# Performance work log

Hardware: AMD Instinct MI355X
Metric: run time of the kernel (lower is better)

The kernel has to match this reference:

```python
import jax, jax.numpy as jnp
import numpy as np

MEAN_LOG = 0.0
STD_LOG = 1.0
D = 32          # context_size (SRU hidden)
K = 64          # num_mix_components
H = 3 * K       # MLP hidden width
LOG_2PI = float(np.log(2.0 * np.pi))


def clamp_preserve_gradients(x, lo, hi):
    # forward clamp, straight-through gradient
    return x + jax.lax.stop_gradient(jnp.clip(x, lo, hi) - x)


def setup_inputs() -> dict:
    key = jax.random.key(0)
    ks = jax.random.split(key, 10)
    B, S = 128, 4096
    inter_times = jax.random.uniform(ks[0], (B, S), dtype=jnp.float32)
    mask = jnp.ones((B, S), dtype=jnp.float32)
    ages_u = jax.random.uniform(ks[1], (B, S), dtype=jnp.float32)
    # SRU parameters (input_size=1, hidden=D, k=4 since 1 != D)
    W = jax.random.normal(ks[2], (1, 4 * D), dtype=jnp.float32) / np.sqrt(1.0)
    v = 0.1 * jax.random.normal(ks[3], (2 * D,), dtype=jnp.float32)   # weight_c (v_f, v_r)
    b = jnp.zeros((2 * D,), dtype=jnp.float32)                         # bias (b_f, b_r)
    context_init = jnp.zeros((D,), dtype=jnp.float32)
    # MLP: (D+1) -> H -> H -> H
    W1 = jax.random.normal(ks[4], (D + 1, H), dtype=jnp.float32) / np.sqrt(D + 1)
    b1 = jnp.zeros((H,), dtype=jnp.float32)
    W2 = jax.random.normal(ks[5], (H, H), dtype=jnp.float32) / np.sqrt(H)
    b2 = jnp.zeros((H,), dtype=jnp.float32)
    W3 = jax.random.normal(ks[6], (H, H), dtype=jnp.float32) / np.sqrt(H)
    b3 = jnp.zeros((H,), dtype=jnp.float32)
    return dict(inter_times=inter_times, mask=mask, ages_u=ages_u, W=W, v=v, b=b,
                context_init=context_init, W1=W1, b1=b1, W2=W2, b2=b2, W3=W3, b3=b3)


def reference(inter_times, mask, ages_u, W, v, b, context_init, W1, b1, W2, b2, W3, b3):
    B, S = inter_times.shape
    # --- features: normalized log inter-event times ---
    feats = (jnp.log(inter_times + 1e-8) - MEAN_LOG) / STD_LOG        # (B,S)
    x = feats[..., None]                                              # (B,S,1)
    # --- SRU: one big input projection, then elementwise recurrence via scan ---
    U = (x @ W).reshape(B, S, 4, D)                                   # (B,S,4,D)
    U = jnp.transpose(U, (1, 0, 2, 3))                                # (S,B,4,D) time-major
    vf, vr = v[:D], v[D:]
    bf, br = b[:D], b[D:]

    def step(c, u):
        u0, u1, u2, u3 = u[:, 0], u[:, 1], u[:, 2], u[:, 3]
        f = jax.nn.sigmoid(u1 + vf * c + bf)
        c_new = f * c + (1.0 - f) * u0
        r = jax.nn.sigmoid(u2 + vr * c_new + br)
        h = r * c_new + (1.0 - r) * u3                                # highway (identity activation)
        return c_new, h

    c0 = jnp.zeros((B, D), dtype=feats.dtype)
    _, hs = jax.lax.scan(step, c0, U)                                 # (S,B,D)
    context = jnp.transpose(hs, (1, 0, 2))                            # (B,S,D)
    # remove_last: shift right, prepend learned init context
    context = jnp.concatenate(
        [jnp.broadcast_to(context_init, (B, 1, D)), context[:, :-1, :]], axis=1)
    # --- age features / residual times ---
    ages = inter_times - inter_times * ages_u                         # elapsed age
    residual_times = inter_times - ages                               # = inter_times * ages_u
    ages_f = (jnp.log(ages + 1e-8) - MEAN_LOG) / STD_LOG
    ctx = jnp.concatenate([context, ages_f[..., None]], axis=-1)      # (B,S,D+1)
    # --- mixture-parameter MLP ---
    h1 = jax.nn.relu(ctx @ W1 + b1)
    h2 = jax.nn.relu(h1 @ W2 + b2)
    raw = h2 @ W3 + b3                                                # (B,S,3K)
    locs = raw[..., :K]
    log_scales = clamp_preserve_gradients(raw[..., K:2 * K], -5.0, 3.0)
    log_w = jax.nn.log_softmax(raw[..., 2 * K:], axis=-1)
    # --- log-normal mixture log-prob ---
    t = jnp.clip(residual_times, 1e-10, None)
    y = jnp.log(t)
    z = (y - MEAN_LOG) / STD_LOG
    zs = (z[..., None] - locs) * jnp.exp(-log_scales)
    comp = log_w - log_scales - 0.5 * LOG_2PI - 0.5 * zs * zs         # (B,S,K)
    log_p = jax.scipy.special.logsumexp(comp, axis=-1) - jnp.log(STD_LOG) - y
    log_p = log_p * mask
    return log_p.sum(-1)                                              # (B,)
```

## Files before the change

### kernel.cpp

```cpp
#include <hip/hip_runtime.h>
#include <hip/hip_bf16.h>
#include <math.h>
#include <type_traits>

#define Bn 128
#define Sn 4096
#define Dn 32
#define Hn 192
#define ASTR 196
#define CH 32
#define CHL 128
#define BURN 128
#define HALF_LOG2PI 0.9189385332046727f

typedef __attribute__((ext_vector_type(8))) short short8v;
typedef __attribute__((ext_vector_type(4))) float f32x4;

__device__ __forceinline__ unsigned short f2bf(float x) {
    return (unsigned short)((__float_as_uint(x) + 0x8000u) >> 16);
}
__device__ __forceinline__ float bf2f(unsigned short u) {
    return __uint_as_float(((unsigned)u) << 16);
}
__device__ __forceinline__ unsigned pack_bf2(float lo, float hi) {
    __hip_bfloat162 h = __float22bfloat162_rn(float2{lo, hi});
    return *reinterpret_cast<unsigned*>(&h);
}

__global__ __launch_bounds__(64) void pack_weights(
    const float* __restrict__ W1, const float* __restrict__ W2,
    const float* __restrict__ W3, unsigned short* __restrict__ wp)
{
    int fid = blockIdx.x, lane = threadIdx.x;
    const float* Wsrc; int Krows, f;
    if (fid < 24)      { Wsrc = W1; Krows = 33;  f = fid; }
    else if (fid < 96) { Wsrc = W2; Krows = 192; f = fid - 24; }
    else               { Wsrc = W3; Krows = 192; f = fid - 96; }
    int kstep = f / 12, nb = f % 12;
    int k0 = kstep * 32 + 8 * (lane >> 4);
    int n  = nb * 16 + (lane & 15);
    short8v v;
#pragma unroll
    for (int j = 0; j < 8; ++j) {
        int k = k0 + j;
        float x = (k < Krows) ? Wsrc[k * Hn + n] : 0.0f;
        v[j] = (short)f2bf(x);
    }
    *(short8v*)(wp + (size_t)fid * 512 + lane * 8) = v;
}

__global__ __launch_bounds__(256) void recurrence_kernel(
    const float* __restrict__ it_g, const float* __restrict__ W,
    const float* __restrict__ v,    const float* __restrict__ bia,
    const float* __restrict__ cinit, unsigned short* __restrict__ ctx)
{
    const float LOG2E = 1.4426950408889634f;
    int g = blockIdx.x * 256 + threadIdx.x;
    int d = g & 31;
    int bc = g >> 5;
    int b = bc & (Bn - 1);
    int chunk = bc >> 7;

    float w0 = W[d], w3 = W[96 + d];
    float nw1l = -W[32 + d] * LOG2E, nw2l = -W[64 + d] * LOG2E;
    float nvfl = -v[d] * LOG2E,      nvrl = -v[32 + d] * LOG2E;
    float nbfl = -bia[d] * LOG2E,    nbrl = -bia[32 + d] * LOG2E;

    const f32x4* itv = (const f32x4*)(it_g + (size_t)b * Sn);
    unsigned short* cp = ctx + ((size_t)b * Sn) * Dn + d;
    int s_start = chunk * CHL;
    int s_end   = s_start + CHL;
    int sbeg    = (chunk == 0) ? 0 : s_start - BURN;
    if (chunk == 0) cp[0] = f2bf(cinit[d]);

    float c = 0.0f;
    int blk0 = sbeg >> 3, blkN = s_end >> 3;
    f32x4 A0 = itv[blk0 * 2], A1 = itv[blk0 * 2 + 1];
    for (int blk = blk0; blk < blkN; ++blk) {
        f32x4 N0 = A0, N1 = A1;
        if (blk + 1 < blkN) { N0 = itv[blk * 2 + 2]; N1 = itv[blk * 2 + 3]; }
        float feat[8];
#pragma unroll
        for (int j = 0; j < 4; ++j) {
            feat[j]     = __logf(A0[j] + 1e-8f);
            feat[j + 4] = __logf(A1[j] + 1e-8f);
        }
        unsigned short hb[8];
#pragma unroll
        for (int j = 0; j < 8; ++j) {
            float ft = feat[j];
            float u0 = ft * w0, u3 = ft * w3;
            float nxfl = fmaf(ft, nw1l, nbfl);
            float nxrl = fmaf(ft, nw2l, nbrl);
            float sfn = fmaf(nvfl, c, nxfl);
            float ef  = __builtin_amdgcn_exp2f(sfn);
            float f_  = __builtin_amdgcn_rcpf(1.0f + ef);
            float cmu = c - u0;
            float cn  = fmaf(f_, cmu, u0);
            float srn = fmaf(nvrl, cn, nxrl);
            float er  = __builtin_amdgcn_exp2f(srn);
            float r_  = __builtin_amdgcn_rcpf(1.0f + er);
            float h   = fmaf(r_, cn - u3, u3);
            c = cn;
            hb[j] = f2bf(h);
        }
        int s0 = blk * 8;
        if (s0 >= s_start) {
#pragma unroll
            for (int j = 0; j < 8; ++j)
                if (s0 + j + 1 < Sn) cp[(size_t)(s0 + j + 1) * Dn] = hb[j];
        }
        A0 = N0; A1 = N1;
    }
}

__global__ __launch_bounds__(128, 2) void mlp_kernel(
    const float* __restrict__ it_g, const float* __restrict__ mask_g,
    const float* __restrict__ au_g, const unsigned short* __restrict__ ctxb,
    const unsigned short* __restrict__ wp,
    const float* __restrict__ b1, const float* __restrict__ b2,
    const float* __restrict__ b3, float* __restrict__ out)
{
    __shared__ __align__(16) unsigned short Acts[64 * ASTR];
    __shared__ float wsum[2];

    const int tid = threadIdx.x;
    const int lane = tid & 63;
    const int wv = tid >> 6;
    const int gq = lane >> 4;
    const int cl = lane & 15;
    const long tile = (long)blockIdx.x * 64;
    const int b = (int)(tile >> 12);
    const int nbase = wv * 6;

    {
        int tok = tid >> 1, h = tid & 1;
        unsigned short* row = Acts + tok * ASTR;
        const unsigned short* src = ctxb + (tile + tok) * Dn + h * 16;
        *(short8v*)(row + h * 16)     = *(const short8v*)src;
        *(short8v*)(row + h * 16 + 8) = *(const short8v*)(src + 8);
        short8v z = {0, 0, 0, 0, 0, 0, 0, 0};
        if (h == 0) {
            float itv = it_g[tile + tok];
            float auv = au_g[tile + tok];
            short8v za = z;
            za[0] = (short)f2bf(__logf(fmaf(-auv, itv, itv) + 1e-8f));
            *(short8v*)(row + 32) = za;
        } else {
            *(short8v*)(row + 40) = z;
            *(short8v*)(row + 48) = z;
            *(short8v*)(row + 56) = z;
        }
    }
    __syncthreads();

    f32x4 acc[6][4];

    auto run_layer = [&](auto NKC, const unsigned short* wpl,
                         const float* __restrict__ bias) {
        constexpr int nk = NKC.value;
#pragma unroll
        for (int j = 0; j < 6; ++j) {
            f32x4 bb = *(const f32x4*)(bias + (nbase + j) * 16 + 4 * gq);
#pragma unroll
            for (int m = 0; m < 4; ++m) acc[j][m] = bb;
        }
#pragma unroll
        for (int ks = 0; ks < nk; ++ks) {
            short8v bfv[4];
#pragma unroll
            for (int m = 0; m < 4; ++m)
                bfv[m] = *(const short8v*)(Acts + (m * 16 + cl) * ASTR + ks * 32 + 8 * gq);
            const unsigned short* wk = wpl + ((size_t)ks * 12 + nbase) * 512 + lane * 8;
#pragma unroll
            for (int j = 0; j < 6; ++j) {
                short8v af = *(const short8v*)(wk + j * 512);
#pragma unroll
                for (int m = 0; m < 4; ++m)
                    acc[j][m] = __builtin_amdgcn_mfma_f32_16x16x32_bf16(af, bfv[m], acc[j][m], 0, 0, 0);
            }
        }
    };

    auto store_h = [&](bool relu) {
#pragma unroll
        for (int j = 0; j < 6; ++j) {
            int fbase = (nbase + j) * 16 + 4 * gq;
#pragma unroll
            for (int m = 0; m < 4; ++m) {
                f32x4 vv = acc[j][m];
                if (relu) {
#pragma unroll
                    for (int r = 0; r < 4; ++r) vv[r] = fmaxf(vv[r], 0.0f);
                }
                uint2 pk;
                pk.x = pack_bf2(vv[0], vv[1]);
                pk.y = pack_bf2(vv[2], vv[3]);
                *(uint2*)(Acts + (m * 16 + cl) * ASTR + fbase) = pk;
            }
        }
    };

    run_layer(std::integral_constant<int, 2>{}, wp, b1);
    __syncthreads();
    store_h(true);
    __syncthreads();
    run_layer(std::integral_constant<int, 6>{}, wp + 24 * 512, b2);
    __syncthreads();
    store_h(true);
    __syncthreads();
    run_layer(std::integral_constant<int, 6>{}, wp + 96 * 512, b3);
    __syncthreads();
    store_h(false);
    __syncthreads();

    float psum = 0.0f;
#pragma unroll
    for (int pass = 0; pass < 2; ++pass) {
        int t = lane >> 2;
        int cpart = lane & 3;
        int rowi = wv * 32 + pass * 16 + t;
        long tok = tile + rowi;
        const unsigned short* rowp = Acts + rowi * ASTR + 16 * cpart;

        short8v L0 = *(const short8v*)(rowp);
        short8v L1 = *(const short8v*)(rowp + 8);
        short8v S0 = *(const short8v*)(rowp + 64);
        short8v S1 = *(const short8v*)(rowp + 72);
        short8v G0 = *(const short8v*)(rowp + 128);
        short8v G1 = *(const short8v*)(rowp + 136);

        float itv = it_g[tok];
        float auv = au_g[tok];
        float mk  = mask_g[tok];
        float y = __logf(fmaxf(itv * auv, 1e-10f));

        float lg[16];
#pragma unroll
        for (int i = 0; i < 8; ++i) {
            lg[i]     = bf2f((unsigned short)G0[i]);
            lg[8 + i] = bf2f((unsigned short)G1[i]);
        }
        float m1 = lg[0];
#pragma unroll
        for (int i = 1; i < 16; ++i) m1 = fmaxf(m1, lg[i]);
        m1 = fmaxf(m1, __shfl_xor(m1, 1, 64));
        m1 = fmaxf(m1, __shfl_xor(m1, 2, 64));

        float sa = 0.0f, sb = 0.0f;
#pragma unroll
        for (int i = 0; i < 16; ++i) {
            float loc = bf2f((unsigned short)(i < 8 ? L0[i] : L1[i - 8]));
            float lsr = bf2f((unsigned short)(i < 8 ? S0[i] : S1[i - 8]));
            lsr = fminf(fmaxf(lsr, -5.0f), 3.0f);
            float zs = (y - loc) * __expf(-lsr);
            float g = -lsr - HALF_LOG2PI - 0.5f * zs * zs;
            sa += __expf(lg[i] - m1);
            sb += __expf(lg[i] - m1 + g);
        }
        sa += __shfl_xor(sa, 1, 64); sa += __shfl_xor(sa, 2, 64);
        sb += __shfl_xor(sb, 1, 64); sb += __shfl_xor(sb, 2, 64);

        float lp = (__logf(sb) - __logf(sa) - y) * mk;
        if (cpart == 0) psum += lp;
    }
#pragma unroll
    for (int mm = 4; mm < 64; mm <<= 1) psum += __shfl_xor(psum, mm, 64);
    psum += __shfl_xor(psum, 1, 64);
    psum += __shfl_xor(psum, 2, 64);
    if (lane == 0) wsum[wv] = psum;
    __syncthreads();
    if (tid == 0) atomicAdd(out + b, wsum[0] + wsum[1]);
}

extern "C" void kernel_launch(void* const* d_in, const int* in_sizes, int n_in,
                              void* d_out, int out_size, void* d_ws, size_t ws_size,
                              hipStream_t stream) {
    const float* it_g  = (const float*)d_in[0];
    const float* mask  = (const float*)d_in[1];
    const float* au    = (const float*)d_in[2];
    const float* W     = (const float*)d_in[3];
    const float* v     = (const float*)d_in[4];
    const float* bia   = (const float*)d_in[5];
    const float* cinit = (const float*)d_in[6];
    const float* W1    = (const float*)d_in[7];
    const float* b1    = (const float*)d_in[8];
    const float* W2    = (const float*)d_in[9];
    const float* b2    = (const float*)d_in[10];
    const float* W3    = (const float*)d_in[11];
    const float* b3    = (const float*)d_in[12];
    float* out = (float*)d_out;

    unsigned short* ctxb = (unsigned short*)d_ws;
    unsigned short* wp   = ctxb + (size_t)Bn * Sn * Dn;

    hipMemsetAsync(d_out, 0, (size_t)out_size * sizeof(float), stream);

    pack_weights<<<168, 64, 0, stream>>>(W1, W2, W3, wp);
    recurrence_kernel<<<(Bn * Dn * CH) / 256, 256, 0, stream>>>(
        it_g, W, v, bia, cinit, ctxb);
    mlp_kernel<<<(Bn * Sn) / 64, 128, 0, stream>>>(
        it_g, mask, au, ctxb, wp, b1, b2, b3, out);
}
```

Measured before the change: 194.1 us.

## Compute mixture log-prob epilogue directly from layer-3 MFMA accumulators

Layer 3's output columns are reassigned across the two waves so each wave holds matching loc, log-scale and weight blocks for the same 32 mixture components in registers. The log-sum-exp then runs straight from the fp32 accumulators, and only the per-wave partial results are merged through a small LDS exchange. This removes the bf16 store of layer-3 outputs to LDS, the barriers around it and the reload. As a side effect, the final mixture parameters are no longer rounded to bf16. The cost is more register pressure and a two-way log-sum-exp merge.

Result: faster. 186.0 us (-4.2%).

```diff
diff --git a/kernel.cpp b/kernel.cpp
--- a/kernel.cpp
+++ b/kernel.cpp
@@ -18,9 +18,6 @@
 
 __device__ __forceinline__ unsigned short f2bf(float x) {
     return (unsigned short)((__float_as_uint(x) + 0x8000u) >> 16);
-}
-__device__ __forceinline__ float bf2f(unsigned short u) {
-    return __uint_as_float(((unsigned)u) << 16);
 }
 __device__ __forceinline__ unsigned pack_bf2(float lo, float hi) {
     __hip_bfloat162 h = __float22bfloat162_rn(float2{lo, hi});
@@ -131,7 +128,8 @@
     const int cl = lane & 15;
     const long tile = (long)blockIdx.x * 64;
     const int b = (int)(tile >> 12);
-    const int nbase = wv * 6;
+
+#define NBM(j) ((j) + (((j) >= 2) ? 2 : 0) + (((j) >= 4) ? 2 : 0) + 2 * wv)
 
     {
         int tok = tid >> 1, h = tid & 1;
@@ -161,7 +159,7 @@
         constexpr int nk = NKC.value;
 #pragma unroll
         for (int j = 0; j < 6; ++j) {
-            f32x4 bb = *(const f32x4*)(bias + (nbase + j) * 16 + 4 * gq);
+            f32x4 bb = *(const f32x4*)(bias + NBM(j) * 16 + 4 * gq);
 #pragma unroll
             for (int m = 0; m < 4; ++m) acc[j][m] = bb;
         }
@@ -171,10 +169,10 @@
 #pragma unroll
             for (int m = 0; m < 4; ++m)
                 bfv[m] = *(const short8v*)(Acts + (m * 16 + cl) * ASTR + ks * 32 + 8 * gq);
-            const unsigned short* wk = wpl + ((size_t)ks * 12 + nbase) * 512 + lane * 8;
+            const unsigned short* wk = wpl + (size_t)ks * (12 * 512) + lane * 8;
 #pragma unroll
             for (int j = 0; j < 6; ++j) {
-                short8v af = *(const short8v*)(wk + j * 512);
+                short8v af = *(const short8v*)(wk + NBM(j) * 512);
 #pragma unroll
                 for (int m = 0; m < 4; ++m)
                     acc[j][m] = __builtin_amdgcn_mfma_f32_16x16x32_bf16(af, bfv[m], acc[j][m], 0, 0, 0);
@@ -182,17 +180,15 @@
         }
     };
 
-    auto store_h = [&](bool relu) {
+    auto store_h = [&]() {
 #pragma unroll
         for (int j = 0; j < 6; ++j) {
-            int fbase = (nbase + j) * 16 + 4 * gq;
+            int fbase = NBM(j) * 16 + 4 * gq;
 #pragma unroll
             for (int m = 0; m < 4; ++m) {
                 f32x4 vv = acc[j][m];
-                if (relu) {
-#pragma unroll
-                    for (int r = 0; r < 4; ++r) vv[r] = fmaxf(vv[r], 0.0f);
-                }
+#pragma unroll
+                for (int r = 0; r < 4; ++r) vv[r] = fmaxf(vv[r], 0.0f);
                 uint2 pk;
                 pk.x = pack_bf2(vv[0], vv[1]);
                 pk.y = pack_bf2(vv[2], vv[3]);
@@ -203,74 +199,84 @@
 
     run_layer(std::integral_constant<int, 2>{}, wp, b1);
     __syncthreads();
-    store_h(true);
+    store_h();
     __syncthreads();
     run_layer(std::integral_constant<int, 6>{}, wp + 24 * 512, b2);
     __syncthreads();
-    store_h(true);
+    store_h();
     __syncthreads();
     run_layer(std::integral_constant<int, 6>{}, wp + 96 * 512, b3);
-    __syncthreads();
-    store_h(false);
-    __syncthreads();
-
-    float psum = 0.0f;
-#pragma unroll
-    for (int pass = 0; pass < 2; ++pass) {
-        int t = lane >> 2;
-        int cpart = lane & 3;
-        int rowi = wv * 32 + pass * 16 + t;
-        long tok = tile + rowi;
-        const unsigned short* rowp = Acts + rowi * ASTR + 16 * cpart;
-
-        short8v L0 = *(const short8v*)(rowp);
-        short8v L1 = *(const short8v*)(rowp + 8);
-        short8v S0 = *(const short8v*)(rowp + 64);
-        short8v S1 = *(const short8v*)(rowp + 72);
-        short8v G0 = *(const short8v*)(rowp + 128);
-        short8v G1 = *(const short8v*)(rowp + 136);
+
+    float lseA[4], lseB[4];
+#pragma unroll
+    for (int m = 0; m < 4; ++m) {
+        long tok = tile + m * 16 + cl;
+        float itv = it_g[tok];
+        float auv = au_g[tok];
+        float y = __logf(fmaxf(itv * auv, 1e-10f));
+
+        float m1 = -1e30f;
+#pragma unroll
+        for (int j = 4; j < 6; ++j)
+#pragma unroll
+            for (int r = 0; r < 4; ++r) m1 = fmaxf(m1, acc[j][m][r]);
+        m1 = fmaxf(m1, __shfl_xor(m1, 16, 64));
+        m1 = fmaxf(m1, __shfl_xor(m1, 32, 64));
+
+        float sa = 0.0f, sb = 0.0f;
+#pragma unroll
+        for (int j = 0; j < 2; ++j) {
+#pragma unroll
+            for (int r = 0; r < 4; ++r) {
+                float loc = acc[j][m][r];
+                float lsr = fminf(fmaxf(acc[2 + j][m][r], -5.0f), 3.0f);
+                float lg  = acc[4 + j][m][r];
+                float zs = (y - loc) * __expf(-lsr);
+                float g = -lsr - HALF_LOG2PI - 0.5f * zs * zs;
+                sa += __expf(lg - m1);
+                sb += __expf(lg - m1 + g);
+            }
+        }
+        sa += __shfl_xor(sa, 16, 64); sa += __shfl_xor(sa, 32, 64);
+        sb += __shfl_xor(sb, 16, 64); sb += __shfl_xor(sb, 32, 64);
+        lseA[m] = m1 + __logf(sa);
+        lseB[m] = m1 + __logf(sb);
+    }
+
+    float* X = (float*)Acts;
+    __syncthreads();
+    if (gq == 0) {
+#pragma unroll
+        for (int m = 0; m < 4; ++m) {
+            float2 pr; pr.x = lseA[m]; pr.y = lseB[m];
+            *(float2*)(X + (m * 16 + cl) * 4 + wv * 2) = pr;
+        }
+    }
+    __syncthreads();
+
+    {
+        int t = wv * 32 + (lane & 31);
+        long tok = tile + t;
+        f32x4 pr = *(const f32x4*)(X + t * 4);
+        float ma = fmaxf(pr[0], pr[2]);
+        float lse_a = ma + __logf(__expf(pr[0] - ma) + __expf(pr[2] - ma));
+        float mb = fmaxf(pr[1], pr[3]);
+        float lse_b = mb + __logf(__expf(pr[1] - mb) + __expf(pr[3] - mb));
 
         float itv = it_g[tok];
         float auv = au_g[tok];
         float mk  = mask_g[tok];
         float y = __logf(fmaxf(itv * auv, 1e-10f));
 
-        float lg[16];
-#pragma unroll
-        for (int i = 0; i < 8; ++i) {
-            lg[i]     = bf2f((unsigned short)G0[i]);
-            lg[8 + i] = bf2f((unsigned short)G1[i]);
-        }
-        float m1 = lg[0];
-#pragma unroll
-        for (int i = 1; i < 16; ++i) m1 = fmaxf(m1, lg[i]);
-        m1 = fmaxf(m1, __shfl_xor(m1, 1, 64));
-        m1 = fmaxf(m1, __shfl_xor(m1, 2, 64));
-
-        float sa = 0.0f, sb = 0.0f;
-#pragma unroll
-        for (int i = 0; i < 16; ++i) {
-            float loc = bf2f((unsigned short)(i < 8 ? L0[i] : L1[i - 8]));
-            float lsr = bf2f((unsigned short)(i < 8 ? S0[i] : S1[i - 8]));
-            lsr = fminf(fmaxf(lsr, -5.0f), 3.0f);
-            float zs = (y - loc) * __expf(-lsr);
-            float g = -lsr - HALF_LOG2PI - 0.5f * zs * zs;
-            sa += __expf(lg[i] - m1);
-            sb += __expf(lg[i] - m1 + g);
-        }
-        sa += __shfl_xor(sa, 1, 64); sa += __shfl_xor(sa, 2, 64);
-        sb += __shfl_xor(sb, 1, 64); sb += __shfl_xor(sb, 2, 64);
-
-        float lp = (__logf(sb) - __logf(sa) - y) * mk;
-        if (cpart == 0) psum += lp;
-    }
-#pragma unroll
-    for (int mm = 4; mm < 64; mm <<= 1) psum += __shfl_xor(psum, mm, 64);
-    psum += __shfl_xor(psum, 1, 64);
-    psum += __shfl_xor(psum, 2, 64);
-    if (lane == 0) wsum[wv] = psum;
+        float lp = (lse_b - lse_a - y) * mk;
+        float psum = (lane < 32) ? lp : 0.0f;
+#pragma unroll
+        for (int mm = 1; mm < 64; mm <<= 1) psum += __shfl_xor(psum, mm, 64);
+        if (lane == 0) wsum[wv] = psum;
+    }
     __syncthreads();
     if (tid == 0) atomicAdd(out + b, wsum[0] + wsum[1]);
+#undef NBM
 }
 
 extern "C" void kernel_launch(void* const* d_in, const int* in_sizes, int n_in,
```
